# Kernel tuning notes

Hardware: AMD Instinct MI355X
Metric: run time of the kernel (lower is better)

## Reference

```python
import jax, jax.numpy as jnp
import numpy as np

EMBED_DIM = 512
NUM_HEADS = 8
HEAD_DIM = EMBED_DIM // NUM_HEADS
SEQ = 1024
BSZ = 8
T1 = 0.6
T2 = 0.4
MAX_NEG = -jnp.finfo(jnp.float32).max


def setup_inputs() -> dict:
    key = jax.random.key(0)
    ks = jax.random.split(key, 10)
    shp = (SEQ, BSZ, EMBED_DIM)
    inv = 1.0 / np.sqrt(EMBED_DIM)
    return {
        "query": jax.random.normal(ks[0], shp, jnp.float32),
        "key": jax.random.normal(ks[1], shp, jnp.float32),
        "value": jax.random.normal(ks[2], shp, jnp.float32),
        "query_sem": jax.random.normal(ks[3], shp, jnp.float32),
        "key_sem": jax.random.normal(ks[4], shp, jnp.float32),
        "sem_map": jax.random.uniform(ks[5], (SEQ, SEQ), jnp.float32),
        "in_proj_weight": jax.random.normal(ks[6], (3 * EMBED_DIM, EMBED_DIM), jnp.float32) * inv,
        "in_proj_bias": jnp.zeros((3 * EMBED_DIM,), jnp.float32),
        "out_proj_weight": jax.random.normal(ks[7], (EMBED_DIM, EMBED_DIM), jnp.float32) * inv,
        "out_proj_bias": jnp.zeros((EMBED_DIM,), jnp.float32),
    }


def _heads(x):
    # [T, B, E] -> [B*H, T, head_dim]
    T, B, E = x.shape
    return jnp.transpose(x.reshape(T, B * NUM_HEADS, HEAD_DIM), (1, 0, 2))


def _attn_path(qx, kx, vx, sem_map, Wi, bi, Wo, bo, ssa):
    # packed in-projection (generic path: q, k, v are distinct tensors)
    Wq, Wk, Wv = jnp.split(Wi, 3, axis=0)
    bq, bk, bv = jnp.split(bi, 3)
    q = _heads(qx @ Wq.T + bq)
    k = _heads(kx @ Wk.T + bk)
    v = _heads(vx @ Wv.T + bv)
    scale = 1.0 / np.sqrt(HEAD_DIM)
    scores = jnp.einsum("bte,bse->bts", q * scale, k)  # [B*H, T, S]
    scores = jnp.where(sem_map[None, :, :] < 0.5, MAX_NEG, scores)
    if ssa:
        # keep only the argmax entry per row, others set to max_neg
        idx = jnp.argmax(scores, axis=-1)  # [B*H, T]
        keep = jnp.arange(scores.shape[-1])[None, None, :] == idx[..., None]
        scores = jnp.where(keep, scores, MAX_NEG)
    w = jax.nn.softmax(scores, axis=-1)
    o = jnp.einsum("bts,bse->bte", w, v)  # [B*H, T, head_dim]
    o = jnp.transpose(o, (1, 0, 2)).reshape(SEQ, BSZ, EMBED_DIM)
    return o @ Wo.T + bo


def reference(query, key, value, query_sem, key_sem, sem_map, in_proj_weight, in_proj_bias, out_proj_weight, out_proj_bias):
    # SCA: semantic q/k attend, style value
    x_sca = _attn_path(query_sem, key_sem, value, sem_map, in_proj_weight, in_proj_bias, out_proj_weight, out_proj_bias, ssa=False)
    # SSA: content/style q/k, hard-argmax sparsified attention
    x_ssa = _attn_path(query, key, value, sem_map, in_proj_weight, in_proj_bias, out_proj_weight, out_proj_bias, ssa=True)
    return T1 * x_sca + T2 * x_ssa
```

## Files before the change

kernel.cpp:

```cpp
#include <hip/hip_runtime.h>
#include <float.h>


namespace {
constexpr int kSeq = 1024;
constexpr int kBsz = 8;
constexpr int kEmb = 512;
constexpr int kHD  = 64;
constexpr float kT1 = 0.6f;
constexpr float kT2 = 0.4f;
constexpr float kScale = 0.125f;
constexpr float kMargin = 0.125f;
constexpr int kCap = 256;
}

typedef short bf16x8 __attribute__((ext_vector_type(8)));
typedef float f32x4  __attribute__((ext_vector_type(4)));

union FragU { uint4 u4; bf16x8 f; uint u[4]; };

__device__ __forceinline__ ushort f2bf(float f) {
  uint u = __float_as_uint(f);
  u += 0x7fff + ((u >> 16) & 1);
  return (ushort)(u >> 16);
}
__device__ __forceinline__ uint pack2(float lo, float hi) {
  return (uint)f2bf(lo) | ((uint)f2bf(hi) << 16);
}
__device__ __forceinline__ float bf2f(uint h) {
  return __uint_as_float(h << 16);
}
__device__ __forceinline__ uint monokey(float v) {
  uint u = __float_as_uint(v);
  return (u & 0x80000000u) ? ~u : (u | 0x80000000u);
}

__global__ void smask_prep(const float* __restrict__ SEM,
                           unsigned long long* __restrict__ SMASK) {
  const int t = blockIdx.x;
  const int w4 = threadIdx.x >> 6;
  const int lane = threadIdx.x & 63;
#pragma unroll
  for (int i = 0; i < 4; ++i) {
    const int word = (w4 << 2) + i;
    const float v = SEM[t * kSeq + (word << 6) + lane];
    unsigned long long m = __ballot(v >= 0.5f);
    if (lane == 0) SMASK[t * 16 + word] = m;
  }
}

__global__ __launch_bounds__(128, 2) void proj_v5(
    const float* __restrict__ Xq, const float* __restrict__ Xk,
    const float* __restrict__ W, const float* __restrict__ bias,
    float* __restrict__ OutQ, float* __restrict__ OutK,
    ushort* __restrict__ ShQ, ushort* __restrict__ ShK)
{
  __shared__ float As[32 * 132];
  __shared__ float Bs[32 * 68];

  const int z = blockIdx.z;
  const float* X = z ? Xk : Xq;
  float* Out = z ? OutK : OutQ;
  ushort* shadow = z ? ShK : ShQ;
  const int woff = z << 9;
  const float sscale = z ? 1.0f : kScale;

  const int mBase = blockIdx.x << 7;
  const int nBase = blockIdx.y << 6;
  const int tid = threadIdx.x;
  const int tx = tid & 7;
  const int my = tid >> 3;
  const int br = tid >> 1, bh = (tid & 1) << 4;

  float acc[8][8];
#pragma unroll
  for (int i = 0; i < 8; ++i)
#pragma unroll
    for (int j = 0; j < 8; ++j) acc[i][j] = 0.f;

  const float* xp = X + (size_t)(mBase + tid) * kEmb;
  const float* wp = W + (size_t)(woff + nBase + br) * kEmb + bh;

  float4 pa[8];
#pragma unroll
  for (int c = 0; c < 8; ++c) pa[c] = ((const float4*)xp)[c];
  float4 pb0 = ((const float4*)wp)[0];
  float4 pb1 = ((const float4*)wp)[1];
  float4 pb2 = ((const float4*)wp)[2];
  float4 pb3 = ((const float4*)wp)[3];

  for (int k0 = 0; k0 < kEmb; k0 += 32) {
    __syncthreads();
    {
#pragma unroll
      for (int c = 0; c < 8; ++c) {
        As[((c << 2) + 0) * 132 + tid] = pa[c].x;
        As[((c << 2) + 1) * 132 + tid] = pa[c].y;
        As[((c << 2) + 2) * 132 + tid] = pa[c].z;
        As[((c << 2) + 3) * 132 + tid] = pa[c].w;
      }
      float bv[16] = {pb0.x, pb0.y, pb0.z, pb0.w, pb1.x, pb1.y, pb1.z, pb1.w,
                      pb2.x, pb2.y, pb2.z, pb2.w, pb3.x, pb3.y, pb3.z, pb3.w};
#pragma unroll
      for (int i = 0; i < 16; ++i) Bs[(bh + i) * 68 + br] = bv[i];
    }
    __syncthreads();

    const int kn = k0 + 32;
    if (kn < kEmb) {
#pragma unroll
      for (int c = 0; c < 8; ++c) pa[c] = ((const float4*)(xp + kn))[c];
      pb0 = ((const float4*)(wp + kn))[0];
      pb1 = ((const float4*)(wp + kn))[1];
      pb2 = ((const float4*)(wp + kn))[2];
      pb3 = ((const float4*)(wp + kn))[3];
    }

#pragma unroll 4
    for (int k = 0; k < 32; ++k) {
      float4 A0 = *(const float4*)&As[k * 132 + (my << 3)];
      float4 A1 = *(const float4*)&As[k * 132 + (my << 3) + 4];
      float4 B0 = *(const float4*)&Bs[k * 68 + (tx << 3)];
      float4 B1 = *(const float4*)&Bs[k * 68 + (tx << 3) + 4];
      float aa[8] = {A0.x, A0.y, A0.z, A0.w, A1.x, A1.y, A1.z, A1.w};
      float bb[8] = {B0.x, B0.y, B0.z, B0.w, B1.x, B1.y, B1.z, B1.w};
#pragma unroll
      for (int i = 0; i < 8; ++i)
#pragma unroll
        for (int j = 0; j < 8; ++j)
          acc[i][j] = fmaf(aa[i], bb[j], acc[i][j]);
    }
  }

#pragma unroll
  for (int i = 0; i < 8; ++i) {
    const int m = mBase + (my << 3) + i;
#pragma unroll
    for (int j = 0; j < 8; ++j) {
      const int n = nBase + (tx << 3) + j;
      const float v = acc[i][j] + bias[woff + n];
      const int oi = (((m & 7) << 3) + (n >> 6)) * (kSeq * kHD) +
                     ((m >> 3) << 6) + (n & 63);
      Out[oi] = v;
      shadow[oi] = f2bf(v * sscale);
    }
  }
}

__global__ __launch_bounds__(256, 2) void gemm_bf16(
    const float* __restrict__ X0, const float* __restrict__ X1,
    const float* __restrict__ X2, const ushort* __restrict__ X16,
    const float* __restrict__ W, const float* __restrict__ bias,
    float* __restrict__ OutF, ushort* __restrict__ Out16,
    int woffBase, int aMode, int outMode, float scale0)
{
  __shared__ uint As[128 * 20];
  __shared__ uint Bs[64 * 20];

  const int z = blockIdx.z;
  const float* X = (z == 0) ? X0 : (z == 1) ? X1 : X2;
  const int woff = woffBase + (z << 9);
  const float scale = (z == 0) ? scale0 : 1.0f;
  const size_t zoff = (size_t)z * ((size_t)kSeq * kBsz * kEmb);

  const int mBase = blockIdx.x << 7;
  const int nBase = blockIdx.y << 6;
  const int tid = threadIdx.x;
  const int w = tid >> 6;
  const int l = tid & 63;
  const int l15 = l & 15;
  const int quad = l >> 4;
  const int wm = w & 1, wn = w >> 1;

  const int srow = tid >> 1;
  const int shalf = tid & 1;

  f32x4 acc[4][2];
#pragma unroll
  for (int mi = 0; mi < 4; ++mi)
#pragma unroll
    for (int ni = 0; ni < 2; ++ni) acc[mi][ni] = (f32x4){0.f, 0.f, 0.f, 0.f};

  uint4 qa0, qa1;
  float4 ra0, ra1, ra2, ra3;
  float4 rb0, rb1, rb2, rb3;

#define GLOAD(kk) do {                                                     \
    if (aMode == 2) {                                                      \
      const uint* src_ = (const uint*)X16 + (size_t)(mBase + srow) * 256 + \
                         ((kk) >> 1) + (shalf << 3);                       \
      qa0 = ((const uint4*)src_)[0];                                       \
      qa1 = ((const uint4*)src_)[1];                                       \
    } else {                                                               \
      const float* xp_ = X + (size_t)(mBase + srow) * kEmb + (kk) +        \
                         (shalf << 4);                                     \
      ra0 = ((const float4*)xp_)[0];                                       \
      ra1 = ((const float4*)xp_)[1];                                       \
      ra2 = ((const float4*)xp_)[2];                                       \
      ra3 = ((const float4*)xp_)[3];                                       \
    }                                                                      \
    if (tid < 128) {                                                       \
      const float* wp_ = W + (size_t)(woff + nBase + srow) * kEmb + (kk) + \
                         (shalf << 4);                                     \
      rb0 = ((const float4*)wp_)[0];                                       \
      rb1 = ((const float4*)wp_)[1];                                       \
      rb2 = ((const float4*)wp_)[2];                                       \
      rb3 = ((const float4*)wp_)[3];                                       \
    }                                                                      \
  } while (0)

  GLOAD(0);

  for (int k0 = 0; k0 < kEmb; k0 += 32) {
    uint4 ah0, ah1, bw0, bw1;
    if (aMode == 2) {
      ah0 = qa0; ah1 = qa1;
    } else {
      ah0 = make_uint4(pack2(ra0.x, ra0.y), pack2(ra0.z, ra0.w),
                       pack2(ra1.x, ra1.y), pack2(ra1.z, ra1.w));
      ah1 = make_uint4(pack2(ra2.x, ra2.y), pack2(ra2.z, ra2.w),
                       pack2(ra3.x, ra3.y), pack2(ra3.z, ra3.w));
    }
    if (tid < 128) {
      bw0 = make_uint4(pack2(rb0.x, rb0.y), pack2(rb0.z, rb0.w),
                       pack2(rb1.x, rb1.y), pack2(rb1.z, rb1.w));
      bw1 = make_uint4(pack2(rb2.x, rb2.y), pack2(rb2.z, rb2.w),
                       pack2(rb3.x, rb3.y), pack2(rb3.z, rb3.w));
    }
    __syncthreads();
    {
      uint* dst = As + srow * 20 + (shalf << 3);
      ((uint4*)dst)[0] = ah0;
      ((uint4*)dst)[1] = ah1;
      if (tid < 128) {
        uint* db = Bs + srow * 20 + (shalf << 3);
        ((uint4*)db)[0] = bw0;
        ((uint4*)db)[1] = bw1;
      }
    }
    __syncthreads();

    if (k0 + 32 < kEmb) GLOAD(k0 + 32);

    FragU aF[4], bF[2];
#pragma unroll
    for (int ni = 0; ni < 2; ++ni)
      bF[ni].u4 = *(const uint4*)(Bs + ((wn << 5) + (ni << 4) + l15) * 20 + (quad << 2));
#pragma unroll
    for (int mi = 0; mi < 4; ++mi)
      aF[mi].u4 = *(const uint4*)(As + ((wm << 6) + (mi << 4) + l15) * 20 + (quad << 2));
#pragma unroll
    for (int mi = 0; mi < 4; ++mi)
#pragma unroll
      for (int ni = 0; ni < 2; ++ni)
        acc[mi][ni] = __builtin_amdgcn_mfma_f32_16x16x32_bf16(
            aF[mi].f, bF[ni].f, acc[mi][ni], 0, 0, 0);
  }
#undef GLOAD

#pragma unroll
  for (int ni = 0; ni < 2; ++ni) {
    const int n = nBase + (wn << 5) + (ni << 4) + l15;
    const float bv = bias[woff + n];
#pragma unroll
    for (int mi = 0; mi < 4; ++mi) {
#pragma unroll
      for (int r = 0; r < 4; ++r) {
        const int m = mBase + (wm << 6) + (mi << 4) + (quad << 2) + r;
        const float v = acc[mi][ni][r] + bv;
        if (outMode == 0) {
          OutF[(size_t)m * kEmb + n] = v;
        } else {
          const int oi = (((m & 7) << 3) + (n >> 6)) * (kSeq * kHD) +
                         ((m >> 3) << 6) + (n & 63);
          Out16[zoff + oi] = f2bf(v * scale);
        }
      }
    }
  }
}

__global__ __launch_bounds__(256, 4) void sca_mfma2(
    const ushort* __restrict__ Q16, const ushort* __restrict__ K16,
    const ushort* __restrict__ V16,
    const unsigned long long* __restrict__ SMASK,
    ushort* __restrict__ MIX16)
{
  __shared__ uint ks[64 * 36];
  __shared__ uint vt[64 * 36];
  __shared__ uint ps[4][16 * 36];

  const int t0  = blockIdx.x << 6;
  const int bh  = blockIdx.y;
  const int tid = threadIdx.x;
  const int w    = tid >> 6;
  const int l    = tid & 63;
  const int l15  = l & 15;
  const int quad = l >> 4;

  const uint* Qu = (const uint*)Q16 + (size_t)bh * (kSeq * 32);
  const uint* Ku = (const uint*)K16 + (size_t)bh * (kSeq * 32);
  const uint* Vu = (const uint*)V16 + (size_t)bh * (kSeq * 32);

  FragU qf0, qf1;
  {
    const uint* qrow = Qu + (size_t)(t0 + (w << 4) + l15) * 32;
    qf0.u4 = *(const uint4*)(qrow + (quad << 2));
    qf1.u4 = *(const uint4*)(qrow + 16 + (quad << 2));
  }

  f32x4 oacc[4];
#pragma unroll
  for (int nt = 0; nt < 4; ++nt) oacc[nt] = (f32x4){0.f, 0.f, 0.f, 0.f};
  float den[4] = {0.f, 0.f, 0.f, 0.f};

  uint* psw = ps[w];

  const int sl = tid >> 2, c = tid & 3;
  const int p = tid >> 3, c7 = tid & 7;

  uint4 pk0 = ((const uint4*)(Ku + (size_t)sl * 32 + (c << 3)))[0];
  uint4 pk1 = ((const uint4*)(Ku + (size_t)sl * 32 + (c << 3)))[1];
  uint4 pv0 = *(const uint4*)(Vu + (size_t)(p << 1) * 32 + (c7 << 2));
  uint4 pv1 = *(const uint4*)(Vu + (size_t)(p << 1) * 32 + (c7 << 2) + 32);

  for (int s0 = 0, tile = 0; s0 < kSeq; s0 += 64, ++tile) {
    __syncthreads();
    {
      uint* dst = ks + sl * 36 + (c << 3);
      ((uint4*)dst)[0] = pk0;
      ((uint4*)dst)[1] = pk1;
    }
    {
      FragU A, B;
      A.u4 = pv0;
      B.u4 = pv1;
      const int Wp = (p + ((c7 & 3) << 2)) & 31;
#pragma unroll
      for (int i = 0; i < 8; ++i) {
        uint ai = (A.u[i >> 1] >> ((i & 1) << 4)) & 0xFFFF;
        uint bi = (B.u[i >> 1] >> ((i & 1) << 4)) & 0xFFFF;
        vt[((c7 << 3) + i) * 36 + Wp] = ai | (bi << 16);
      }
    }
    __syncthreads();

    if (s0 + 64 < kSeq) {
      const uint* kp = Ku + (size_t)(s0 + 64 + sl) * 32 + (c << 3);
      pk0 = ((const uint4*)kp)[0];
      pk1 = ((const uint4*)kp)[1];
      const uint* va = Vu + (size_t)(s0 + 64 + (p << 1)) * 32 + (c7 << 2);
      pv0 = *(const uint4*)va;
      pv1 = *(const uint4*)(va + 32);
    }

    unsigned long long wv[4];
#pragma unroll
    for (int r = 0; r < 4; ++r)
      wv[r] = SMASK[(size_t)(t0 + (w << 4) + (quad << 2) + r) * 16 + tile];

#pragma unroll
    for (int st = 0; st < 4; ++st) {
      f32x4 sacc = (f32x4){0.f, 0.f, 0.f, 0.f};
      const int srow = (st << 4) + l15;
      FragU kf0, kf1;
      kf0.u4 = *(const uint4*)(ks + srow * 36 + (quad << 2));
      kf1.u4 = *(const uint4*)(ks + srow * 36 + 16 + (quad << 2));
      sacc = __builtin_amdgcn_mfma_f32_16x16x32_bf16(qf0.f, kf0.f, sacc, 0, 0, 0);
      sacc = __builtin_amdgcn_mfma_f32_16x16x32_bf16(qf1.f, kf1.f, sacc, 0, 0, 0);

#pragma unroll
      for (int r = 0; r < 4; ++r) {
        const int trow = (quad << 2) + r;
        const uint bit = (uint)(wv[r] >> ((st << 4) + l15)) & 1u;
        const float val = bit ? __expf(sacc[r]) : 0.f;
        den[r] += val;
        const int W  = (st << 3) + (l15 >> 1);
        const int Wp = (W + (((trow >> 3) & 1) << 3)) & 31;
        ushort* p16 = (ushort*)(psw + trow * 36 + Wp);
        p16[l15 & 1] = f2bf(val);
      }
    }
#pragma unroll
    for (int ch = 0; ch < 2; ++ch) {
      FragU pf;
      const int pw = ((ch << 4) + (quad << 2) + (((l15 >> 3) & 1) << 3)) & 31;
      pf.u4 = *(const uint4*)(psw + l15 * 36 + pw);
#pragma unroll
      for (int nt = 0; nt < 4; ++nt) {
        const int d = (nt << 4) + l15;
        const int vw = ((ch << 4) + (quad << 2) + (((d >> 3) & 3) << 2)) & 31;
        FragU vf;
        vf.u4 = *(const uint4*)(vt + d * 36 + vw);
        oacc[nt] = __builtin_amdgcn_mfma_f32_16x16x32_bf16(pf.f, vf.f, oacc[nt], 0, 0, 0);
      }
    }
  }

#pragma unroll
  for (int r = 0; r < 4; ++r) {
    float d = den[r];
    d += __shfl_xor(d, 1);
    d += __shfl_xor(d, 2);
    d += __shfl_xor(d, 4);
    d += __shfl_xor(d, 8);
    den[r] = kT1 / d;
  }
  const int b = bh >> 3, h = bh & 7;
#pragma unroll
  for (int nt = 0; nt < 4; ++nt) {
#pragma unroll
    for (int r = 0; r < 4; ++r) {
      const int t = t0 + (w << 4) + (quad << 2) + r;
      const int d = (nt << 4) + l15;
      MIX16[(size_t)(t * kBsz + b) * kEmb + (h << 6) + d] =
          f2bf(oacc[nt][r] * den[r]);
    }
  }
}

__global__ __launch_bounds__(512, 2) void ssa_v3(
    const ushort* __restrict__ Q16, const ushort* __restrict__ K16,
    const float* __restrict__ Qf, const float* __restrict__ Kf,
    const ushort* __restrict__ V16,
    const unsigned long long* __restrict__ SMASK,
    ushort* __restrict__ MIX16)
{
  __shared__ uint ks[64 * 36];
  __shared__ uint2 list[8][kCap];
  __shared__ float thrL[8][16];
  __shared__ unsigned long long key64L[8][16];
  __shared__ uint cnt[8];

  const int t0  = blockIdx.x << 7;
  const int bh  = blockIdx.y;
  const int tid = threadIdx.x;
  const int w    = tid >> 6;
  const int l    = tid & 63;
  const int l15  = l & 15;
  const int quad = l >> 4;

  if (tid < 8) cnt[tid] = 0;
  if (tid < 128) ((unsigned long long*)key64L)[tid] = 0ull;

  const uint* Qu = (const uint*)Q16 + (size_t)bh * (kSeq * 32);
  const uint* Ku = (const uint*)K16 + (size_t)bh * (kSeq * 32);

  FragU qf0, qf1;
  {
    const uint* qrow = Qu + (size_t)(t0 + (w << 4) + l15) * 32;
    qf0.u4 = *(const uint4*)(qrow + (quad << 2));
    qf1.u4 = *(const uint4*)(qrow + 16 + (quad << 2));
  }

  float m4[4] = {-FLT_MAX, -FLT_MAX, -FLT_MAX, -FLT_MAX};

  const int krow = tid >> 3, kc = tid & 7;
  uint4 pk = *(const uint4*)(Ku + (size_t)krow * 32 + (kc << 2));

  for (int s0 = 0, tile = 0; s0 < kSeq; s0 += 64, ++tile) {
    __syncthreads();
    *(uint4*)(ks + krow * 36 + (kc << 2)) = pk;
    __syncthreads();

    if (s0 + 64 < kSeq)
      pk = *(const uint4*)(Ku + (size_t)(s0 + 64 + krow) * 32 + (kc << 2));

    unsigned long long wv[4];
#pragma unroll
    for (int r = 0; r < 4; ++r)
      wv[r] = SMASK[(size_t)(t0 + (w << 4) + (quad << 2) + r) * 16 + tile];

    f32x4 sv[4];
#pragma unroll
    for (int st = 0; st < 4; ++st) {
      f32x4 sacc = (f32x4){0.f, 0.f, 0.f, 0.f};
      const int srow = (st << 4) + l15;
      FragU kf0, kf1;
      kf0.u4 = *(const uint4*)(ks + srow * 36 + (quad << 2));
      kf1.u4 = *(const uint4*)(ks + srow * 36 + 16 + (quad << 2));
      sacc = __builtin_amdgcn_mfma_f32_16x16x32_bf16(qf0.f, kf0.f, sacc, 0, 0, 0);
      sacc = __builtin_amdgcn_mfma_f32_16x16x32_bf16(qf1.f, kf1.f, sacc, 0, 0, 0);
      sv[st] = sacc;
#pragma unroll
      for (int r = 0; r < 4; ++r) {
        const uint bit = (uint)(wv[r] >> ((st << 4) + l15)) & 1u;
        if (bit) m4[r] = fmaxf(m4[r], sacc[r]);
      }
    }
#pragma unroll
    for (int r = 0; r < 4; ++r) {
      float m = m4[r];
      m = fmaxf(m, __shfl_xor(m, 1));
      m = fmaxf(m, __shfl_xor(m, 2));
      m = fmaxf(m, __shfl_xor(m, 4));
      m = fmaxf(m, __shfl_xor(m, 8));
      m4[r] = m;
    }
#pragma unroll
    for (int st = 0; st < 4; ++st) {
#pragma unroll
      for (int r = 0; r < 4; ++r) {
        const uint bit = (uint)(wv[r] >> ((st << 4) + l15)) & 1u;
        const float x = sv[st][r];
        if (bit && x >= m4[r] - kMargin) {
          uint idx = atomicAdd(&cnt[w], 1u);
          if (idx < (uint)kCap) {
            const int rowid = (quad << 2) + r;
            const int s = s0 + (st << 4) + l15;
            list[w][idx] = make_uint2(__float_as_uint(x),
                                      ((uint)rowid << 10) | (uint)s);
          }
        }
      }
    }
  }

  if (l15 == 0) {
#pragma unroll
    for (int r = 0; r < 4; ++r) thrL[w][(quad << 2) + r] = m4[r] - kMargin;
  }
  __syncthreads();

  const uint n = min(cnt[w], (uint)kCap);
  const float* Qbf = Qf + (size_t)bh * (kSeq * kHD);
  const float* Kbf = Kf + (size_t)bh * (kSeq * kHD);
  for (uint base = 0; base < n; base += 64) {
    const uint e = base + (uint)l;
    if (e < n) {
      const uint2 ent = list[w][e];
      const uint rowid = ent.y >> 10;
      const uint s = ent.y & 1023u;
      const float xv = __uint_as_float(ent.x);
      if (xv >= thrL[w][rowid]) {
        const int t = t0 + (w << 4) + (int)rowid;
        const float* qe = Qbf + (size_t)t * kHD;
        const float* ke = Kbf + (size_t)s * kHD;
        float p0 = 0.f, p1 = 0.f, p2 = 0.f, p3 = 0.f;
#pragma unroll
        for (int i = 0; i < 16; ++i) {
          float4 qq = *(const float4*)(qe + (i << 2));
          float4 kk = *(const float4*)(ke + (i << 2));
          p0 = fmaf(qq.x, kk.x, p0);
          p1 = fmaf(qq.y, kk.y, p1);
          p2 = fmaf(qq.z, kk.z, p2);
          p3 = fmaf(qq.w, kk.w, p3);
        }
        const float acc = ((p0 + p1) + (p2 + p3)) * kScale;
        const unsigned long long key =
            ((unsigned long long)monokey(acc) << 16) |
            (unsigned long long)(1023u - s);
        atomicMax(&key64L[w][rowid], key);
      }
    }
  }
  __syncthreads();

  const int b = bh >> 3, h = bh & 7;
  const uint* Vu = (const uint*)V16 + (size_t)bh * (kSeq * 32);
#pragma unroll
  for (int r = 0; r < 4; ++r) {
    const int rowid = (quad << 2) + r;
    const unsigned long long key = key64L[w][rowid];
    const uint s = 1023u - (uint)(key & 0xFFFFull);
    const uint2 vv = *(const uint2*)(Vu + (size_t)s * 32 + (l15 << 1));
    const int t = t0 + (w << 4) + rowid;
    uint* op = (uint*)MIX16 + ((size_t)(t * kBsz + b) * kEmb + (h << 6)) / 2 + (l15 << 1);
    uint2 o = *(uint2*)op;
    float o0 = bf2f(o.x & 0xFFFF) + kT2 * bf2f(vv.x & 0xFFFF);
    float o1 = bf2f(o.x >> 16)    + kT2 * bf2f(vv.x >> 16);
    float o2 = bf2f(o.y & 0xFFFF) + kT2 * bf2f(vv.y & 0xFFFF);
    float o3 = bf2f(o.y >> 16)    + kT2 * bf2f(vv.y >> 16);
    *(uint2*)op = make_uint2(pack2(o0, o1), pack2(o2, o3));
  }
}

extern "C" void kernel_launch(void* const* d_in, const int* in_sizes, int n_in,
                              void* d_out, int out_size, void* d_ws, size_t ws_size,
                              hipStream_t stream) {
  const float* query  = (const float*)d_in[0];
  const float* key    = (const float*)d_in[1];
  const float* value  = (const float*)d_in[2];
  const float* qsem   = (const float*)d_in[3];
  const float* ksem   = (const float*)d_in[4];
  const float* semmap = (const float*)d_in[5];
  const float* Wi     = (const float*)d_in[6];
  const float* bi     = (const float*)d_in[7];
  const float* Wo     = (const float*)d_in[8];
  const float* bo     = (const float*)d_in[9];
  float* out = (float*)d_out;

  char* ws = (char*)d_ws;
  unsigned long long* SMASK = (unsigned long long*)ws;          ws += 1024 * 16 * 8;
  ushort* Q16  = (ushort*)ws;  ws += (size_t)64 * kSeq * kHD * 2;
  ushort* K16  = (ushort*)ws;  ws += (size_t)64 * kSeq * kHD * 2;
  ushort* V16  = (ushort*)ws;  ws += (size_t)64 * kSeq * kHD * 2;
  ushort* MIX16 = (ushort*)ws; ws += (size_t)kSeq * kBsz * kEmb * 2;
  float* P1 = (float*)ws;      ws += (size_t)64 * kSeq * kHD * 4;
  float* P0 = out;

  const dim3 gp(64, 8, 2);
  const dim3 g3(64, 8, 3);
  const dim3 gb(64, 8);
  const dim3 gs(16, 64);
  const dim3 gv(8, 64);

  smask_prep<<<1024, 256, 0, stream>>>(semmap, SMASK);
  gemm_bf16<<<g3, 256, 0, stream>>>(qsem, ksem, value, nullptr, Wi, bi,
                                    nullptr, Q16, 0, 0, 1, kScale);
  sca_mfma2<<<gs, 256, 0, stream>>>(Q16, K16, V16, SMASK, MIX16);
  proj_v5<<<gp, 128, 0, stream>>>(query, key, Wi, bi, P0, P1, Q16, K16);
  ssa_v3<<<gv, 512, 0, stream>>>(Q16, K16, P0, P1, V16, SMASK, MIX16);
  gemm_bf16<<<gb, 256, 0, stream>>>(nullptr, nullptr, nullptr, MIX16, Wo, bo,
                                    out, nullptr, 0, 2, 0, 1.0f);
}
```

Baseline: 415.6 us.

## Restructure fp32 Q/K projection to stage only X in LDS and stream weights from registers

The fp32 projection kernel for the SSA path is rewritten. It uses 256 threads and a 128x32 output tile, so the grid doubles along N. Only the X tile goes to shared memory; each wave reads its 8 weight rows straight from global memory into registers and software-pipelines the next slice, and each lane computes 2 rows x 8 columns. This drops the shared-memory B tile and its transpose stores and raises the thread count. In exchange, weight data is re-read from global/L2 by more blocks and per-thread arithmetic intensity is lower.

```diff
diff --git a/kernel.cpp b/kernel.cpp
--- a/kernel.cpp
+++ b/kernel.cpp
@@ -49,14 +49,13 @@
   }
 }
 
-__global__ __launch_bounds__(128, 2) void proj_v5(
+__global__ __launch_bounds__(256, 2) void proj_v6(
     const float* __restrict__ Xq, const float* __restrict__ Xk,
     const float* __restrict__ W, const float* __restrict__ bias,
     float* __restrict__ OutQ, float* __restrict__ OutK,
     ushort* __restrict__ ShQ, ushort* __restrict__ ShK)
 {
-  __shared__ float As[32 * 132];
-  __shared__ float Bs[32 * 68];
+  __shared__ float As[128 * 36];
 
   const int z = blockIdx.z;
   const float* X = z ? Xk : Xq;
@@ -66,79 +65,91 @@
   const float sscale = z ? 1.0f : kScale;
 
   const int mBase = blockIdx.x << 7;
-  const int nBase = blockIdx.y << 6;
+  const int nBase = blockIdx.y << 5;
   const int tid = threadIdx.x;
-  const int tx = tid & 7;
-  const int my = tid >> 3;
-  const int br = tid >> 1, bh = (tid & 1) << 4;
-
-  float acc[8][8];
-#pragma unroll
-  for (int i = 0; i < 8; ++i)
-#pragma unroll
-    for (int j = 0; j < 8; ++j) acc[i][j] = 0.f;
-
-  const float* xp = X + (size_t)(mBase + tid) * kEmb;
-  const float* wp = W + (size_t)(woff + nBase + br) * kEmb + bh;
-
-  float4 pa[8];
-#pragma unroll
-  for (int c = 0; c < 8; ++c) pa[c] = ((const float4*)xp)[c];
-  float4 pb0 = ((const float4*)wp)[0];
-  float4 pb1 = ((const float4*)wp)[1];
-  float4 pb2 = ((const float4*)wp)[2];
-  float4 pb3 = ((const float4*)wp)[3];
+  const int l   = tid & 63;
+  const int wq  = __builtin_amdgcn_readfirstlane(tid >> 6);
+
+  const int ar = tid >> 1;
+  const int ah = (tid & 1) << 4;
+
+  const float* xp = X + (size_t)(mBase + ar) * kEmb + ah;
+  const float* Wp = W + (size_t)(woff + nBase + (wq << 3)) * kEmb;
+
+  float acc[2][8];
+#pragma unroll
+  for (int r = 0; r < 2; ++r)
+#pragma unroll
+    for (int c = 0; c < 8; ++c) acc[r][c] = 0.f;
+
+  float4 bcur[8], bnxt[8];
+#pragma unroll
+  for (int c = 0; c < 8; ++c) bcur[c] = *(const float4*)(Wp + c * kEmb);
+#pragma unroll
+  for (int c = 0; c < 8; ++c) bnxt[c] = bcur[c];
+
+  const int rowA = l * 36;
+  const int rowB = (l + 64) * 36;
 
   for (int k0 = 0; k0 < kEmb; k0 += 32) {
+    float4 s0 = ((const float4*)(xp + k0))[0];
+    float4 s1 = ((const float4*)(xp + k0))[1];
+    float4 s2 = ((const float4*)(xp + k0))[2];
+    float4 s3 = ((const float4*)(xp + k0))[3];
     __syncthreads();
     {
-#pragma unroll
-      for (int c = 0; c < 8; ++c) {
-        As[((c << 2) + 0) * 132 + tid] = pa[c].x;
-        As[((c << 2) + 1) * 132 + tid] = pa[c].y;
-        As[((c << 2) + 2) * 132 + tid] = pa[c].z;
-        As[((c << 2) + 3) * 132 + tid] = pa[c].w;
-      }
-      float bv[16] = {pb0.x, pb0.y, pb0.z, pb0.w, pb1.x, pb1.y, pb1.z, pb1.w,
-                      pb2.x, pb2.y, pb2.z, pb2.w, pb3.x, pb3.y, pb3.z, pb3.w};
-#pragma unroll
-      for (int i = 0; i < 16; ++i) Bs[(bh + i) * 68 + br] = bv[i];
-    }
-    __syncthreads();
-
-    const int kn = k0 + 32;
-    if (kn < kEmb) {
-#pragma unroll
-      for (int c = 0; c < 8; ++c) pa[c] = ((const float4*)(xp + kn))[c];
-      pb0 = ((const float4*)(wp + kn))[0];
-      pb1 = ((const float4*)(wp + kn))[1];
-      pb2 = ((const float4*)(wp + kn))[2];
-      pb3 = ((const float4*)(wp + kn))[3];
-    }
-
-#pragma unroll 4
-    for (int k = 0; k < 32; ++k) {
-      float4 A0 = *(const float4*)&As[k * 132 + (my << 3)];
-      float4 A1 = *(const float4*)&As[k * 132 + (my << 3) + 4];
-      float4 B0 = *(const float4*)&Bs[k * 68 + (tx << 3)];
-      float4 B1 = *(const float4*)&Bs[k * 68 + (tx << 3) + 4];
-      float aa[8] = {A0.x, A0.y, A0.z, A0.w, A1.x, A1.y, A1.z, A1.w};
-      float bb[8] = {B0.x, B0.y, B0.z, B0.w, B1.x, B1.y, B1.z, B1.w};
-#pragma unroll
-      for (int i = 0; i < 8; ++i)
-#pragma unroll
-        for (int j = 0; j < 8; ++j)
-          acc[i][j] = fmaf(aa[i], bb[j], acc[i][j]);
-    }
-  }
-
-#pragma unroll
-  for (int i = 0; i < 8; ++i) {
-    const int m = mBase + (my << 3) + i;
-#pragma unroll
-    for (int j = 0; j < 8; ++j) {
-      const int n = nBase + (tx << 3) + j;
-      const float v = acc[i][j] + bias[woff + n];
+      float* dst = &As[ar * 36 + ah];
+      *(float4*)(dst + 0)  = s0;
+      *(float4*)(dst + 4)  = s1;
+      *(float4*)(dst + 8)  = s2;
+      *(float4*)(dst + 12) = s3;
+    }
+    __syncthreads();
+
+    float4 a0c = *(const float4*)&As[rowA];
+    float4 a1c = *(const float4*)&As[rowB];
+    float4 a0n = a0c, a1n = a1c;
+
+#pragma unroll
+    for (int g = 0; g < 8; ++g) {
+      if (g < 7) {
+        a0n = *(const float4*)&As[rowA + ((g + 1) << 2)];
+        a1n = *(const float4*)&As[rowB + ((g + 1) << 2)];
+#pragma unroll
+        for (int c = 0; c < 8; ++c)
+          bnxt[c] = *(const float4*)(Wp + c * kEmb + k0 + ((g + 1) << 2));
+      } else if (k0 + 32 < kEmb) {
+#pragma unroll
+        for (int c = 0; c < 8; ++c)
+          bnxt[c] = *(const float4*)(Wp + c * kEmb + k0 + 32);
+      }
+#pragma unroll
+      for (int kk = 0; kk < 4; ++kk) {
+        const float a0 = kk == 0 ? a0c.x : kk == 1 ? a0c.y
+                       : kk == 2 ? a0c.z : a0c.w;
+        const float a1 = kk == 0 ? a1c.x : kk == 1 ? a1c.y
+                       : kk == 2 ? a1c.z : a1c.w;
+#pragma unroll
+        for (int c = 0; c < 8; ++c) {
+          const float bv = kk == 0 ? bcur[c].x : kk == 1 ? bcur[c].y
+                         : kk == 2 ? bcur[c].z : bcur[c].w;
+          acc[0][c] = fmaf(a0, bv, acc[0][c]);
+          acc[1][c] = fmaf(a1, bv, acc[1][c]);
+        }
+      }
+      a0c = a0n; a1c = a1n;
+#pragma unroll
+      for (int c = 0; c < 8; ++c) bcur[c] = bnxt[c];
+    }
+  }
+
+#pragma unroll
+  for (int r = 0; r < 2; ++r) {
+    const int m = mBase + (r << 6) + l;
+#pragma unroll
+    for (int c = 0; c < 8; ++c) {
+      const int n = nBase + (wq << 3) + c;
+      const float v = acc[r][c] + bias[woff + n];
       const int oi = (((m & 7) << 3) + (n >> 6)) * (kSeq * kHD) +
                      ((m >> 3) << 6) + (n & 63);
       Out[oi] = v;
@@ -599,7 +610,7 @@
   float* P1 = (float*)ws;      ws += (size_t)64 * kSeq * kHD * 4;
   float* P0 = out;
 
-  const dim3 gp(64, 8, 2);
+  const dim3 gp(64, 16, 2);
   const dim3 g3(64, 8, 3);
   const dim3 gb(64, 8);
   const dim3 gs(16, 64);
@@ -609,7 +620,7 @@
   gemm_bf16<<<g3, 256, 0, stream>>>(qsem, ksem, value, nullptr, Wi, bi,
                                     nullptr, Q16, 0, 0, 1, kScale);
   sca_mfma2<<<gs, 256, 0, stream>>>(Q16, K16, V16, SMASK, MIX16);
-  proj_v5<<<gp, 128, 0, stream>>>(query, key, Wi, bi, P0, P1, Q16, K16);
+  proj_v6<<<gp, 256, 0, stream>>>(query, key, Wi, bi, P0, P1, Q16, K16);
   ssa_v3<<<gv, 512, 0, stream>>>(Q16, K16, P0, P1, V16, SMASK, MIX16);
   gemm_bf16<<<gb, 256, 0, stream>>>(nullptr, nullptr, nullptr, MIX16, Wo, bo,
                                     out, nullptr, 0, 2, 0, 1.0f);
```

Result: slower. 558.3 us (+34.3%).
